# Kernel optimization log

Measured on AMD Instinct MI355X. Metric: run time of the kernel, lower is better.

## Reference

```python
import jax, jax.numpy as jnp
import numpy as np

B, H, W, C = 16, 64, 64, 512
NH, WS, SS = 16, 8, 4
HD = C // NH
N = WS * WS
MLP = 4 * C
EPS = 1e-5


def window_partition(x, ws):
    b, h, w, c = x.shape
    x = x.reshape(b, h // ws, ws, w // ws, ws, c).transpose(0, 1, 3, 2, 4, 5)
    return x.reshape(-1, ws, ws, c)


def window_reverse(win, ws, h, w):
    c = win.shape[-1]
    x = win.reshape(-1, h // ws, w // ws, ws, ws, c).transpose(0, 1, 3, 2, 4, 5)
    return x.reshape(-1, h, w, c)


def _rel_pos_index():
    coords = np.stack(np.meshgrid(np.arange(WS), np.arange(WS), indexing='ij'))  # [2,WS,WS]
    cf = coords.reshape(2, -1)
    rc = (cf[:, :, None] - cf[:, None, :]).transpose(1, 2, 0)  # [N,N,2]
    rc[:, :, 0] += WS - 1
    rc[:, :, 1] += WS - 1
    rc[:, :, 0] *= 2 * WS - 1
    return jnp.asarray(rc.sum(-1), dtype=jnp.int32)  # [N,N]


def _attn_mask():
    # region ids for shifted windows (HF get_attn_mask)
    img = np.zeros((1, H, W, 1), dtype=np.float32)
    slices = (slice(0, -WS), slice(-WS, -SS), slice(-SS, None))
    cnt = 0
    for hs in slices:
        for ws_ in slices:
            img[:, hs, ws_, :] = cnt
            cnt += 1
    mw = np.asarray(window_partition(jnp.asarray(img), WS)).reshape(-1, N)  # [nw,N]
    mask = mw[:, None, :] - mw[:, :, None]
    mask = np.where(mask != 0, -100.0, 0.0).astype(np.float32)
    return jnp.asarray(mask)  # [nw,N,N]


REL_IDX = _rel_pos_index()
ATTN_MASK = _attn_mask()


def layer_norm(x, g, b):
    mu = x.mean(-1, keepdims=True)
    var = ((x - mu) ** 2).mean(-1, keepdims=True)
    return (x - mu) * jax.lax.rsqrt(var + EPS) * g + b


def setup_inputs() -> dict:
    key = jax.random.key(0)
    ks = jax.random.split(key, 16)
    s = 0.02
    return {
        'hidden_states': jax.random.normal(ks[0], (B, H * W, C), jnp.float32),
        'q_w': jax.random.normal(ks[1], (C, C), jnp.float32) * s,
        'q_b': jnp.zeros((C,), jnp.float32),
        'k_w': jax.random.normal(ks[2], (C, C), jnp.float32) * s,
        'k_b': jnp.zeros((C,), jnp.float32),
        'v_w': jax.random.normal(ks[3], (C, C), jnp.float32) * s,
        'v_b': jnp.zeros((C,), jnp.float32),
        'proj_w': jax.random.normal(ks[4], (C, C), jnp.float32) * s,
        'proj_b': jnp.zeros((C,), jnp.float32),
        'rel_bias_table': jax.random.normal(ks[5], ((2 * WS - 1) * (2 * WS - 1), NH), jnp.float32) * s,
        'ln1_w': jnp.ones((C,), jnp.float32),
        'ln1_b': jnp.zeros((C,), jnp.float32),
        'ln2_w': jnp.ones((C,), jnp.float32),
        'ln2_b': jnp.zeros((C,), jnp.float32),
        'fc1_w': jax.random.normal(ks[6], (MLP, C), jnp.float32) * s,
        'fc1_b': jnp.zeros((MLP,), jnp.float32),
        'fc2_w': jax.random.normal(ks[7], (C, MLP), jnp.float32) * s,
        'fc2_b': jnp.zeros((C,), jnp.float32),
    }


def reference(hidden_states, q_w, q_b, k_w, k_b, v_w, v_b, proj_w, proj_b,
              rel_bias_table, ln1_w, ln1_b, ln2_w, ln2_b, fc1_w, fc1_b, fc2_w, fc2_b):
    shortcut = hidden_states
    x = layer_norm(hidden_states, ln1_w, ln1_b).reshape(B, H, W, C)
    # cyclic shift
    x = jnp.roll(x, (-SS, -SS), axis=(1, 2))
    win = window_partition(x, WS).reshape(-1, N, C)  # [B*nw, N, C]
    Bw = win.shape[0]

    def heads(t):  # [Bw,N,C] -> [Bw,NH,N,HD]
        return t.reshape(Bw, N, NH, HD).transpose(0, 2, 1, 3)

    q = heads(win @ q_w.T + q_b)
    k = heads(win @ k_w.T + k_b)
    v = heads(win @ v_w.T + v_b)

    scores = jnp.einsum('bhnd,bhmd->bhnm', q, k) / jnp.sqrt(jnp.float32(HD))
    bias = rel_bias_table[REL_IDX.reshape(-1)].reshape(N, N, NH).transpose(2, 0, 1)  # [NH,N,N]
    scores = scores + bias[None]
    nw = ATTN_MASK.shape[0]
    scores = scores.reshape(Bw // nw, nw, NH, N, N) + ATTN_MASK[None, :, None]
    scores = scores.reshape(Bw, NH, N, N)
    probs = jax.nn.softmax(scores, axis=-1)
    ctx = jnp.einsum('bhnm,bhmd->bhnd', probs, v).transpose(0, 2, 1, 3).reshape(Bw, N, C)
    attn_out = ctx @ proj_w.T + proj_b

    shifted = window_reverse(attn_out.reshape(-1, WS, WS, C), WS, H, W)
    x = jnp.roll(shifted, (SS, SS), axis=(1, 2)).reshape(B, H * W, C)
    h = shortcut + x

    y = layer_norm(h, ln2_w, ln2_b)
    y = jax.nn.gelu(y @ fc1_w.T + fc1_b, approximate=False)
    y = y @ fc2_w.T + fc2_b
    return h + y
```

## Files before the change

kernel.cpp:

```cpp
#include <hip/hip_runtime.h>
#include <cmath>
#include <cstdint>
#include <cstddef>

typedef __bf16 bf16;
typedef __bf16 bf16x8 __attribute__((ext_vector_type(8)));
typedef float f32x4 __attribute__((ext_vector_type(4)));

#define DEVINL __device__ __forceinline__

DEVINL void gload_lds16(const bf16* g, bf16* l) {
    __builtin_amdgcn_global_load_lds(
        (const __attribute__((address_space(1))) void*)g,
        (__attribute__((address_space(3))) void*)l,
        16, 0, 0);
}

DEVINL bool probe_f32(const uint32_t* probe) { return *probe == 0x3F800000u; }

#define OFF_QW  0u
#define OFF_KW  262144u
#define OFF_VW  524288u
#define OFF_PW  786432u
#define OFF_F1W 1048576u
#define OFF_F2W 2097152u
#define OFF_REL 3145728u
#define OFF_QB  3149328u
#define OFF_KB  3149840u
#define OFF_VB  3150352u
#define OFF_PB  3150864u
#define OFF_L1W 3151376u
#define OFF_L1B 3151888u
#define OFF_L2W 3152400u
#define OFF_L2B 3152912u
#define OFF_F1B 3153424u
#define OFF_F2B 3155472u
#define PRM_TOT 3155984u

struct P17 { const void* p[17]; };

__global__ __launch_bounds__(256) void conv_params(P17 ps, const uint32_t* probe,
                                                   bf16* __restrict__ dst) {
    const size_t off[18] = {OFF_QW, OFF_KW, OFF_VW, OFF_PW, OFF_F1W, OFF_F2W,
                            OFF_REL, OFF_QB, OFF_KB, OFF_VB, OFF_PB, OFF_L1W,
                            OFF_L1B, OFF_L2W, OFF_L2B, OFF_F1B, OFF_F2B, PRM_TOT};
    size_t e = ((size_t)blockIdx.x * 256 + threadIdx.x) * 8;
    if (e >= PRM_TOT) return;
    int s = 0;
#pragma unroll
    for (int i = 1; i < 17; ++i) s = (e >= off[i]) ? i : s;
    const size_t loc = e - off[s];
    if (probe_f32(probe)) {
        const float* sp = (const float*)ps.p[s] + loc;
        bf16x8 o;
#pragma unroll
        for (int t = 0; t < 8; ++t) o[t] = (bf16)sp[t];
        *(bf16x8*)(dst + e) = o;
    } else {
        *(bf16x8*)(dst + e) = *(const bf16x8*)((const bf16*)ps.p[s] + loc);
    }
}

template <int MODE>
__global__ __launch_bounds__(256) void ln_kernel(const void* __restrict__ src0,
                                                 const uint32_t* __restrict__ probe,
                                                 const float* __restrict__ srcf,
                                                 const bf16* __restrict__ g,
                                                 const bf16* __restrict__ bb,
                                                 bf16* __restrict__ out,
                                                 bf16* __restrict__ hidC,
                                                 size_t base_elt) {
    const int row = blockIdx.x * 4 + (threadIdx.x >> 6);
    const int lane = threadIdx.x & 63;
    size_t srow;
    if (MODE == 0) {
        int win = row >> 6, t = row & 63;
        int b = win >> 6, wi = win & 63;
        int hs = ((wi >> 3) << 3) + (t >> 3);
        int ws = ((wi & 7) << 3) + (t & 7);
        srow = (size_t)b * 4096 + (size_t)((hs + 4) & 63) * 64 + ((ws + 4) & 63);
    } else {
        srow = row;
    }
    float x[8];
    if (MODE == 0) {
        bf16x8 cv;
        if (probe_f32(probe)) {
            const float* sp = (const float*)src0 + base_elt + srow * 512 + lane * 8;
            const f32x4* p = (const f32x4*)sp;
            f32x4 a = p[0], c = p[1];
#pragma unroll
            for (int t = 0; t < 4; ++t) { x[t] = a[t]; x[4 + t] = c[t]; }
#pragma unroll
            for (int t = 0; t < 8; ++t) cv[t] = (bf16)x[t];
        } else {
            cv = *(const bf16x8*)((const bf16*)src0 + base_elt + srow * 512 + lane * 8);
#pragma unroll
            for (int t = 0; t < 8; ++t) x[t] = (float)cv[t];
        }
        *(bf16x8*)(hidC + srow * 512 + lane * 8) = cv;
    } else {
        const f32x4* p = (const f32x4*)(srcf + srow * 512 + lane * 8);
        f32x4 a = p[0], c = p[1];
#pragma unroll
        for (int t = 0; t < 4; ++t) { x[t] = a[t]; x[4 + t] = c[t]; }
    }
    float s = 0.f, s2 = 0.f;
#pragma unroll
    for (int t = 0; t < 8; ++t) { s += x[t]; s2 += x[t] * x[t]; }
    for (int off = 1; off < 64; off <<= 1) {
        s += __shfl_xor(s, off, 64);
        s2 += __shfl_xor(s2, off, 64);
    }
    const float mu = s * (1.0f / 512.0f);
    const float var = s2 * (1.0f / 512.0f) - mu * mu;
    const float rs = rsqrtf(var + 1e-5f);
    bf16x8 gg = *(const bf16x8*)(g + lane * 8);
    bf16x8 bv = *(const bf16x8*)(bb + lane * 8);
    bf16x8 o;
#pragma unroll
    for (int t = 0; t < 8; ++t)
        o[t] = (bf16)(((x[t] - mu) * rs) * (float)gg[t] + (float)bv[t]);
    *(bf16x8*)(out + (size_t)row * 512 + lane * 8) = o;
}

template <int N, int K, int EPI>
__global__ __launch_bounds__(256) void gemm_bt(const bf16* __restrict__ A,
                                               const bf16* __restrict__ W,
                                               const bf16* __restrict__ bias,
                                               void* __restrict__ outp,
                                               const bf16* __restrict__ auxb,
                                               const float* __restrict__ auxf,
                                               size_t obase,
                                               const uint32_t* probe) {
    static_assert(K % 64 == 0, "K must be a multiple of 64");
    static_assert(N % 128 == 0, "N must be a multiple of 128");
    __shared__ __align__(16) char sA[16384];
    __shared__ __align__(16) char sB[16384];
    const int tid = threadIdx.x;
    constexpr int NBN = N / 128;
    const int nwg = (int)gridDim.x;
    const int bid = (int)blockIdx.x;
    const int swz = (bid & 7) * (nwg >> 3) + (bid >> 3);
    const int bm = swz / NBN, bn = swz % NBN;

    const int wave = tid >> 6, lane = tid & 63;
    const int wm = (wave >> 1) << 6, wn = (wave & 1) << 6;
    const int lrow = lane & 15, quad = lane >> 4;

    const uint32_t rsw = (uint32_t)(lrow & 7) << 4;
    const uint32_t cb0 = ((uint32_t)(quad * 16)) ^ rsw;
    const uint32_t cb1 = ((uint32_t)(quad * 16 + 64)) ^ rsw;
    const int sswz = (tid & 56) << 1;
    const uint32_t arow = (uint32_t)(wm + lrow) * 128u;
    const uint32_t brow = (uint32_t)(wn + lrow) * 128u;

    bool f32o = false;
    if constexpr (EPI == 3) f32o = probe_f32(probe);

    f32x4 acc[4][4] = {};
    const bf16* Ab = A + (size_t)bm * 128 * K;
    const bf16* Wb = W + (size_t)bn * 128 * K;

    for (int k0 = 0; k0 < K; k0 += 64) {
#pragma unroll
        for (int r = 0; r < 4; ++r) {
            const int X = r * 4096 + tid * 16;
            const int sx = X ^ sswz;
            const int row = sx >> 7, col = (sx & 127) >> 1;
            gload_lds16(Ab + (size_t)row * K + k0 + col, (bf16*)(sA + X));
            gload_lds16(Wb + (size_t)row * K + k0 + col, (bf16*)(sB + X));
        }
        __syncthreads();
        bf16x8 af[4][2], bfr[4][2];
#pragma unroll
        for (int i = 0; i < 4; ++i) {
            af[i][0]  = *(const bf16x8*)(sA + (arow + i * 2048 + cb0));
            af[i][1]  = *(const bf16x8*)(sA + (arow + i * 2048 + cb1));
            bfr[i][0] = *(const bf16x8*)(sB + (brow + i * 2048 + cb0));
            bfr[i][1] = *(const bf16x8*)(sB + (brow + i * 2048 + cb1));
        }
#pragma unroll
        for (int i = 0; i < 4; ++i)
#pragma unroll
            for (int j = 0; j < 4; ++j)
#pragma unroll
                for (int ks = 0; ks < 2; ++ks)
                    acc[i][j] = __builtin_amdgcn_mfma_f32_16x16x32_bf16(
                        af[i][ks], bfr[j][ks], acc[i][j], 0, 0, 0);
        __syncthreads();
    }

#pragma unroll
    for (int i = 0; i < 4; ++i) {
#pragma unroll
        for (int r = 0; r < 4; ++r) {
            const int m = bm * 128 + wm + i * 16 + quad * 4 + r;
            size_t dest = 0;
            if (EPI == 1) {
                int win = m >> 6, t = m & 63;
                int b = win >> 6, wi = win & 63;
                int hs = ((wi >> 3) << 3) + (t >> 3);
                int ws = ((wi & 7) << 3) + (t & 7);
                dest = (size_t)b * 4096 + (size_t)((hs + 4) & 63) * 64 + ((ws + 4) & 63);
            }
#pragma unroll
            for (int j = 0; j < 4; ++j) {
                const int n = bn * 128 + wn + j * 16 + lrow;
                float v = acc[i][j][r] + (float)bias[n];
                if (EPI == 0) {
                    ((bf16*)outp)[(size_t)m * N + n] = (bf16)v;
                } else if (EPI == 1) {
                    ((float*)outp)[dest * 512 + n] = v + (float)auxb[dest * 512 + n];
                } else if (EPI == 2) {
                    float gl = 0.5f * v * (1.0f + erff(v * 0.70710678118654752f));
                    ((bf16*)outp)[(size_t)m * N + n] = (bf16)gl;
                } else {
                    float o = v + auxf[(size_t)m * N + n];
                    if (f32o) ((float*)outp)[obase + (size_t)m * N + n] = o;
                    else      ((bf16*)outp)[obase + (size_t)m * N + n] = (bf16)o;
                }
            }
        }
    }
}

__global__ __launch_bounds__(256) void attn_kernel(const bf16* __restrict__ qkv,
                                                   const bf16* __restrict__ table,
                                                   bf16* __restrict__ ctx) {
    __shared__ bf16 sVt[4][32 * 64];
    __shared__ bf16 sP[4][64 * 64];
    const int win = blockIdx.x;
    const int wave = threadIdx.x >> 6, lane = threadIdx.x & 63;
    const int head = blockIdx.y * 4 + wave;
    const int lrow = lane & 15, quad = lane >> 4;
    const size_t baseq = (size_t)win * 64 * 1536 + head * 32;
    const size_t basec = (size_t)win * 64 * 512 + head * 32;

    {
        const bf16* vr = qkv + baseq + 1024 + (size_t)lane * 1536;
#pragma unroll
        for (int d0 = 0; d0 < 32; d0 += 8) {
            bf16x8 vv = *(const bf16x8*)(vr + d0);
#pragma unroll
            for (int t = 0; t < 8; ++t) sVt[wave][(d0 + t) * 64 + lane] = vv[t];
        }
    }

    f32x4 sacc[4][4] = {};
    {
        bf16x8 qa[4], kb[4];
#pragma unroll
        for (int i = 0; i < 4; ++i)
            qa[i] = *(const bf16x8*)(qkv + baseq + (size_t)(i * 16 + lrow) * 1536 + quad * 8);
#pragma unroll
        for (int j = 0; j < 4; ++j)
            kb[j] = *(const bf16x8*)(qkv + baseq + 512 + (size_t)(j * 16 + lrow) * 1536 + quad * 8);
#pragma unroll
        for (int i = 0; i < 4; ++i)
#pragma unroll
            for (int j = 0; j < 4; ++j)
                sacc[i][j] = __builtin_amdgcn_mfma_f32_16x16x32_bf16(qa[i], kb[j], sacc[i][j], 0, 0, 0);
    }

    const int wi = win & 63;
    const int hb8 = (wi >> 3) << 3, wb8 = (wi & 7) << 3;
    const float scale = 0.17677669529663689f;
#pragma unroll
    for (int ti = 0; ti < 4; ++ti) {
#pragma unroll
        for (int r = 0; r < 4; ++r) {
            const int i = ti * 16 + quad * 4 + r;
            const int ih = i >> 3, iw = i & 7;
            const int ah = hb8 + ih, aw = wb8 + iw;
            const int rgi = ((ah < 56) ? 0 : (ah < 60) ? 1 : 2) * 3 +
                            ((aw < 56) ? 0 : (aw < 60) ? 1 : 2);
            float rowmax = -1e30f;
#pragma unroll
            for (int tj = 0; tj < 4; ++tj) {
                const int j = tj * 16 + lrow;
                const int jh = j >> 3, jw = j & 7;
                const int bh = hb8 + jh, bw = wb8 + jw;
                const int rgj = ((bh < 56) ? 0 : (bh < 60) ? 1 : 2) * 3 +
                                ((bw < 56) ? 0 : (bw < 60) ? 1 : 2);
                const int ridx = (ih - jh + 7) * 15 + (iw - jw + 7);
                float sv = sacc[ti][tj][r] * scale + (float)table[ridx * 16 + head] +
                           ((rgi == rgj) ? 0.0f : -100.0f);
                sacc[ti][tj][r] = sv;
                rowmax = fmaxf(rowmax, sv);
            }
            for (int off = 1; off < 16; off <<= 1)
                rowmax = fmaxf(rowmax, __shfl_xor(rowmax, off, 64));
            float rsum = 0.f;
#pragma unroll
            for (int tj = 0; tj < 4; ++tj) {
                float e = __expf(sacc[ti][tj][r] - rowmax);
                sacc[ti][tj][r] = e;
                rsum += e;
            }
            for (int off = 1; off < 16; off <<= 1) rsum += __shfl_xor(rsum, off, 64);
            const float inv = 1.0f / rsum;
#pragma unroll
            for (int tj = 0; tj < 4; ++tj)
                sP[wave][(size_t)i * 64 + tj * 16 + lrow] = (bf16)(sacc[ti][tj][r] * inv);
        }
    }
    __syncthreads();

    f32x4 cacc[4][2] = {};
#pragma unroll
    for (int ks = 0; ks < 2; ++ks) {
        bf16x8 vbf[2];
#pragma unroll
        for (int tn = 0; tn < 2; ++tn)
            vbf[tn] = *(const bf16x8*)&sVt[wave][(tn * 16 + lrow) * 64 + ks * 32 + quad * 8];
#pragma unroll
        for (int mi = 0; mi < 4; ++mi) {
            bf16x8 pa = *(const bf16x8*)&sP[wave][(size_t)(mi * 16 + lrow) * 64 + ks * 32 + quad * 8];
#pragma unroll
            for (int tn = 0; tn < 2; ++tn)
                cacc[mi][tn] = __builtin_amdgcn_mfma_f32_16x16x32_bf16(pa, vbf[tn], cacc[mi][tn], 0, 0, 0);
        }
    }
#pragma unroll
    for (int mi = 0; mi < 4; ++mi)
#pragma unroll
        for (int tn = 0; tn < 2; ++tn)
#pragma unroll
            for (int r = 0; r < 4; ++r) {
                const int i = mi * 16 + quad * 4 + r;
                const int d = tn * 16 + lrow;
                ctx[basec + (size_t)i * 512 + d] = (bf16)cacc[mi][tn][r];
            }
}

extern "C" void kernel_launch(void* const* d_in, const int* in_sizes, int n_in,
                              void* d_out, int out_size, void* d_ws, size_t ws_size,
                              hipStream_t stream) {
    (void)in_sizes; (void)n_in; (void)out_size;
    const uint32_t* probe = (const uint32_t*)d_in[10];
    char* ws = (char*)d_ws;
    const size_t MB = (size_t)1 << 20;

    bf16* prm = (bf16*)ws;
    P17 ps;
    ps.p[0] = d_in[1];  ps.p[1] = d_in[3];  ps.p[2] = d_in[5];  ps.p[3] = d_in[7];
    ps.p[4] = d_in[14]; ps.p[5] = d_in[16]; ps.p[6] = d_in[9];  ps.p[7] = d_in[2];
    ps.p[8] = d_in[4];  ps.p[9] = d_in[6];  ps.p[10] = d_in[8]; ps.p[11] = d_in[10];
    ps.p[12] = d_in[11]; ps.p[13] = d_in[12]; ps.p[14] = d_in[13];
    ps.p[15] = d_in[15]; ps.p[16] = d_in[17];
    conv_params<<<dim3((PRM_TOT / 8 + 255) / 256), dim3(256), 0, stream>>>(ps, probe, prm);

    int nb = 1;
    for (int c = 16; c >= 2; c >>= 1)
        if (8 * MB + (size_t)c * 36 * MB <= ws_size) { nb = c; break; }
    const size_t R = (size_t)nb * 4096;
    char* arena = ws + 8 * MB;
    bf16* hidC = (bf16*)(arena);
    bf16* Xc   = (bf16*)(arena + 1024 * R);
    bf16* qkv  = (bf16*)(arena + 2048 * R);
    float* hc  = (float*)(arena + 5120 * R);
    bf16* a1   = (bf16*)(arena + 7168 * R);

    const int nchunks = 16 / nb;
    const size_t Mh = R / 2;

    for (int cb = 0; cb < nchunks; ++cb) {
        ln_kernel<0><<<dim3((unsigned)(R / 4)), dim3(256), 0, stream>>>(
            d_in[0], probe, nullptr, prm + OFF_L1W, prm + OFF_L1B, Xc, hidC,
            (size_t)cb * R * 512);

        gemm_bt<1536, 512, 0><<<dim3((unsigned)(R / 128) * 12), dim3(256), 0, stream>>>(
            Xc, prm + OFF_QW, prm + OFF_QB, qkv, nullptr, nullptr, 0, nullptr);

        attn_kernel<<<dim3((unsigned)(R / 64), 4), dim3(256), 0, stream>>>(
            qkv, prm + OFF_REL, Xc);

        gemm_bt<512, 512, 1><<<dim3((unsigned)(R / 128) * 4), dim3(256), 0, stream>>>(
            Xc, prm + OFF_PW, prm + OFF_PB, hc, hidC, nullptr, 0, nullptr);

        ln_kernel<1><<<dim3((unsigned)(R / 4)), dim3(256), 0, stream>>>(
            nullptr, nullptr, hc, prm + OFF_L2W, prm + OFF_L2B, Xc, nullptr, 0);

        for (int hf = 0; hf < 2; ++hf) {
            gemm_bt<2048, 512, 2><<<dim3((unsigned)(Mh / 128) * 16), dim3(256), 0, stream>>>(
                Xc + (size_t)hf * Mh * 512, prm + OFF_F1W, prm + OFF_F1B, a1,
                nullptr, nullptr, 0, nullptr);
            gemm_bt<512, 2048, 3><<<dim3((unsigned)(Mh / 128) * 4), dim3(256), 0, stream>>>(
                a1, prm + OFF_F2W, prm + OFF_F2B, d_out,
                nullptr, hc + (size_t)hf * Mh * 512,
                ((size_t)cb * R + (size_t)hf * Mh) * 512, probe);
        }
    }
}
```

Measured before the change: 1.181 ms.

## Double-buffer GEMM LDS tiles and run MLP on the full chunk

The GEMM K loop now uses two LDS buffers per operand. The next K-tile's global-to-LDS loads are issued before the MFMAs on the current tile, so memory latency overlaps compute and one barrier per iteration is dropped. The workspace is re-laid out so qkv and the fc1 activation share one region, which lowers the per-chunk footprint. That allows larger chunks and lets the fc1/fc2 GEMMs run over the whole chunk instead of two halves, meaning fewer, larger launches. LDS use per block doubles to 64 KB, which may lower occupancy.

```diff
diff --git a/kernel.cpp b/kernel.cpp
--- a/kernel.cpp
+++ b/kernel.cpp
@@ -135,8 +135,8 @@
                                                const uint32_t* probe) {
     static_assert(K % 64 == 0, "K must be a multiple of 64");
     static_assert(N % 128 == 0, "N must be a multiple of 128");
-    __shared__ __align__(16) char sA[16384];
-    __shared__ __align__(16) char sB[16384];
+    __shared__ __align__(16) char sA[2][16384];
+    __shared__ __align__(16) char sB[2][16384];
     const int tid = threadIdx.x;
     constexpr int NBN = N / 128;
     const int nwg = (int)gridDim.x;
@@ -162,23 +162,37 @@
     const bf16* Ab = A + (size_t)bm * 128 * K;
     const bf16* Wb = W + (size_t)bn * 128 * K;
 
-    for (int k0 = 0; k0 < K; k0 += 64) {
-#pragma unroll
-        for (int r = 0; r < 4; ++r) {
-            const int X = r * 4096 + tid * 16;
-            const int sx = X ^ sswz;
-            const int row = sx >> 7, col = (sx & 127) >> 1;
-            gload_lds16(Ab + (size_t)row * K + k0 + col, (bf16*)(sA + X));
-            gload_lds16(Wb + (size_t)row * K + k0 + col, (bf16*)(sB + X));
-        }
-        __syncthreads();
+#pragma unroll
+    for (int r = 0; r < 4; ++r) {
+        const int X = r * 4096 + tid * 16;
+        const int sx = X ^ sswz;
+        const int row = sx >> 7, col = (sx & 127) >> 1;
+        gload_lds16(Ab + (size_t)row * K + col, (bf16*)(sA[0] + X));
+        gload_lds16(Wb + (size_t)row * K + col, (bf16*)(sB[0] + X));
+    }
+    __syncthreads();
+
+    constexpr int NT = K / 64;
+    int p = 0;
+    for (int t = 0; t < NT - 1; ++t) {
         bf16x8 af[4][2], bfr[4][2];
 #pragma unroll
         for (int i = 0; i < 4; ++i) {
-            af[i][0]  = *(const bf16x8*)(sA + (arow + i * 2048 + cb0));
-            af[i][1]  = *(const bf16x8*)(sA + (arow + i * 2048 + cb1));
-            bfr[i][0] = *(const bf16x8*)(sB + (brow + i * 2048 + cb0));
-            bfr[i][1] = *(const bf16x8*)(sB + (brow + i * 2048 + cb1));
+            af[i][0]  = *(const bf16x8*)(sA[p] + (arow + i * 2048 + cb0));
+            af[i][1]  = *(const bf16x8*)(sA[p] + (arow + i * 2048 + cb1));
+            bfr[i][0] = *(const bf16x8*)(sB[p] + (brow + i * 2048 + cb0));
+            bfr[i][1] = *(const bf16x8*)(sB[p] + (brow + i * 2048 + cb1));
+        }
+        {
+            const int k0 = (t + 1) * 64;
+#pragma unroll
+            for (int r = 0; r < 4; ++r) {
+                const int X = r * 4096 + tid * 16;
+                const int sx = X ^ sswz;
+                const int row = sx >> 7, col = (sx & 127) >> 1;
+                gload_lds16(Ab + (size_t)row * K + k0 + col, (bf16*)(sA[p ^ 1] + X));
+                gload_lds16(Wb + (size_t)row * K + k0 + col, (bf16*)(sB[p ^ 1] + X));
+            }
         }
 #pragma unroll
         for (int i = 0; i < 4; ++i)
@@ -189,6 +203,25 @@
                     acc[i][j] = __builtin_amdgcn_mfma_f32_16x16x32_bf16(
                         af[i][ks], bfr[j][ks], acc[i][j], 0, 0, 0);
         __syncthreads();
+        p ^= 1;
+    }
+    {
+        bf16x8 af[4][2], bfr[4][2];
+#pragma unroll
+        for (int i = 0; i < 4; ++i) {
+            af[i][0]  = *(const bf16x8*)(sA[p] + (arow + i * 2048 + cb0));
+            af[i][1]  = *(const bf16x8*)(sA[p] + (arow + i * 2048 + cb1));
+            bfr[i][0] = *(const bf16x8*)(sB[p] + (brow + i * 2048 + cb0));
+            bfr[i][1] = *(const bf16x8*)(sB[p] + (brow + i * 2048 + cb1));
+        }
+#pragma unroll
+        for (int i = 0; i < 4; ++i)
+#pragma unroll
+            for (int j = 0; j < 4; ++j)
+#pragma unroll
+                for (int ks = 0; ks < 2; ++ks)
+                    acc[i][j] = __builtin_amdgcn_mfma_f32_16x16x32_bf16(
+                        af[i][ks], bfr[j][ks], acc[i][j], 0, 0, 0);
     }
 
 #pragma unroll
@@ -353,17 +386,16 @@
 
     int nb = 1;
     for (int c = 16; c >= 2; c >>= 1)
-        if (8 * MB + (size_t)c * 36 * MB <= ws_size) { nb = c; break; }
+        if (8 * MB + (size_t)c * 32 * MB <= ws_size) { nb = c; break; }
     const size_t R = (size_t)nb * 4096;
     char* arena = ws + 8 * MB;
     bf16* hidC = (bf16*)(arena);
     bf16* Xc   = (bf16*)(arena + 1024 * R);
-    bf16* qkv  = (bf16*)(arena + 2048 * R);
-    float* hc  = (float*)(arena + 5120 * R);
-    bf16* a1   = (bf16*)(arena + 7168 * R);
+    float* hc  = (float*)(arena + 2048 * R);
+    bf16* qkv  = (bf16*)(arena + 4096 * R);
+    bf16* a1   = (bf16*)(arena + 4096 * R);
 
     const int nchunks = 16 / nb;
-    const size_t Mh = R / 2;
 
     for (int cb = 0; cb < nchunks; ++cb) {
         ln_kernel<0><<<dim3((unsigned)(R / 4)), dim3(256), 0, stream>>>(
@@ -382,14 +414,10 @@
         ln_kernel<1><<<dim3((unsigned)(R / 4)), dim3(256), 0, stream>>>(
             nullptr, nullptr, hc, prm + OFF_L2W, prm + OFF_L2B, Xc, nullptr, 0);
 
-        for (int hf = 0; hf < 2; ++hf) {
-            gemm_bt<2048, 512, 2><<<dim3((unsigned)(Mh / 128) * 16), dim3(256), 0, stream>>>(
-                Xc + (size_t)hf * Mh * 512, prm + OFF_F1W, prm + OFF_F1B, a1,
-                nullptr, nullptr, 0, nullptr);
-            gemm_bt<512, 2048, 3><<<dim3((unsigned)(Mh / 128) * 4), dim3(256), 0, stream>>>(
-                a1, prm + OFF_F2W, prm + OFF_F2B, d_out,
-                nullptr, hc + (size_t)hf * Mh * 512,
-                ((size_t)cb * R + (size_t)hf * Mh) * 512, probe);
-        }
-    }
-}
+        gemm_bt<2048, 512, 2><<<dim3((unsigned)(R / 128) * 16), dim3(256), 0, stream>>>(
+            Xc, prm + OFF_F1W, prm + OFF_F1B, a1, nullptr, nullptr, 0, nullptr);
+        gemm_bt<512, 2048, 3><<<dim3((unsigned)(R / 128) * 4), dim3(256), 0, stream>>>(
+            a1, prm + OFF_F2W, prm + OFF_F2B, d_out,
+            nullptr, hc, (size_t)cb * R * 512, probe);
+    }
+}
```

After: 1.180 ms. No clear change (-0.1%).
